# Optimization experiments

Hardware: AMD Instinct MI355X
Metric: run time of the kernel (lower is better)

Reference implementation:

```python
import jax, jax.numpy as jnp
import numpy as np
from jax import lax

DN = ('NCHW', 'OIHW', 'NCHW')


def convbn(x, w, s, b, relu=True):
    # conv (no bias) + folded BatchNorm affine (+ optional ReLU)
    y = lax.conv_general_dilated(x, w, (1, 1), 'SAME', dimension_numbers=DN)
    y = y * s[None, :, None, None] + b[None, :, None, None]
    return jnp.maximum(y, 0.0) if relu else y


_PARAM_SHAPES = [
    ('t', (128, 256, 3, 3)), ('l', (128, 256, 3, 3)),
    ('b', (128, 256, 3, 3)), ('r', (128, 256, 3, 3)),
    ('tl3', (256, 128, 3, 3)), ('br3', (256, 128, 3, 3)),
    ('tl1', (256, 256, 1, 1)), ('br1', (256, 256, 1, 1)),
    ('tlo', (256, 256, 3, 3)), ('bro', (256, 256, 3, 3)),
]


def setup_inputs() -> dict:
    key = jax.random.key(0)
    B, C, H, W = 8, 256, 128, 128
    ks = jax.random.split(key, 3 * len(_PARAM_SHAPES) + 1)
    inp = {'x': jax.random.normal(ks[0], (B, C, H, W), jnp.float32)}
    i = 1
    for name, shape in _PARAM_SHAPES:
        cout = shape[0]
        inp['w_' + name] = jax.random.normal(ks[i], shape, jnp.float32) * 0.05
        inp['s_' + name] = 1.0 + 0.1 * jax.random.normal(ks[i + 1], (cout,), jnp.float32)
        inp['b_' + name] = 0.1 * jax.random.normal(ks[i + 2], (cout,), jnp.float32)
        i += 3
    return inp


def reference(x, w_t, s_t, b_t, w_l, s_l, b_l, w_b, s_b, b_b, w_r, s_r, b_r,
              w_tl3, s_tl3, b_tl3, w_br3, s_br3, b_br3,
              w_tl1, s_tl1, b_tl1, w_br1, s_br1, b_br1,
              w_tlo, s_tlo, b_tlo, w_bro, s_bro, b_bro):
    # directional corner pools = (reverse-)cummax along H (axis 2) or W (axis 3)
    t = convbn(x, w_t, s_t, b_t)
    tp = lax.cummax(t, axis=2, reverse=True)   # top_pool: max over rows >= h
    l = convbn(x, w_l, s_l, b_l)
    lp = lax.cummax(l, axis=3, reverse=True)   # left_pool: max over cols >= w
    bo = convbn(x, w_b, s_b, b_b)
    bp = lax.cummax(bo, axis=2)                # bottom_pool: max over rows <= h
    r = convbn(x, w_r, s_r, b_r)
    rp = lax.cummax(r, axis=3)                 # right_pool: max over cols <= w

    tl = convbn(tp + lp, w_tl3, s_tl3, b_tl3, relu=False)
    tl = jnp.maximum(tl + convbn(x, w_tl1, s_tl1, b_tl1, relu=False), 0.0)
    out_tl = convbn(tl, w_tlo, s_tlo, b_tlo)

    br = convbn(bp + rp, w_br3, s_br3, b_br3, relu=False)
    br = jnp.maximum(br + convbn(x, w_br1, s_br1, b_br1, relu=False), 0.0)
    out_br = convbn(br, w_bro, s_bro, b_bro)
    return out_tl, out_br
```

## Files before the change

### kernel.cpp

```cpp
#include <hip/hip_runtime.h>
#include <cstdint>
#include <cstddef>


typedef float  f32x4 __attribute__((ext_vector_type(4)));
typedef float  f4v   __attribute__((ext_vector_type(4)));
typedef short  s16x8 __attribute__((ext_vector_type(8)));
typedef unsigned short u16x4 __attribute__((ext_vector_type(4)));

__device__ __forceinline__ float bf2f(unsigned short u) {
    unsigned x = ((unsigned)u) << 16;
    return __builtin_bit_cast(float, x);
}
__device__ __forceinline__ unsigned short f2bf(float f) {
    unsigned u = __builtin_bit_cast(unsigned, f);
    unsigned r = (u + 0x7fffu + ((u >> 16) & 1u)) >> 16;
    return (unsigned short)r;
}

#define GL_LDS(gp, lp) __builtin_amdgcn_global_load_lds( \
    (const __attribute__((address_space(1))) unsigned int*)(const void*)(gp), \
    (__attribute__((address_space(3))) unsigned int*)(void*)(lp), 16, 0, 0)

template<int CIN, int COUT, bool RELU, bool OUTF32>
__global__ __launch_bounds__(256, 4)
void conv3_mfma(const unsigned short* __restrict__ in,
                const unsigned short* __restrict__ wpk,
                const float* __restrict__ sc, const float* __restrict__ bi,
                void* __restrict__ outv)
{
    __shared__ unsigned short lds[2][8704];
    const int tid  = threadIdx.x;
    const int lane = tid & 63;
    const int wv   = tid >> 6;
    const int c    = lane & 15;
    const int g    = lane >> 4;
    const int gx     = blockIdx.x;
    const int wtile  = gx & 1;
    const int octile = gx >> 1;
    const int h0   = blockIdx.y * 2;
    const int n    = blockIdx.z;
    const int w0   = wtile * 64;
    const int r    = wv >> 1;
    const int ocbase = octile * 128 + (wv & 1) * 64;
    const int ocf0   = octile * 8 + (wv & 1) * 4;

    int addrB[3];
    #pragma unroll
    for (int kx = 0; kx < 3; ++kx) {
        int ps0 = c + kx;
        addrB[kx] = r * 4224 + ps0 * 64 + ((g ^ ((ps0 >> 1) & 3)) << 4);
    }

    int so[5];
    #pragma unroll
    for (int it = 0; it < 5; ++it) {
        int u   = it * 256 + tid;
        int row = u / 264;
        int rem = u - row * 264;
        int ps  = rem >> 2;
        int s   = rem & 3;
        int icq = s ^ ((ps >> 1) & 3);
        so[it] = ((n * 130 + h0 + row) * 130 + (w0 + ps)) * CIN + icq * 8;
    }

    auto STAGE = [&](int chunk, int bsel) {
        const unsigned short* bp = in + chunk * 32;
        char* lb = (char*)lds + bsel * 17408 + tid * 16;
        #pragma unroll
        for (int it = 0; it < 4; ++it)
            GL_LDS(bp + so[it], lb + it * 4096);
        if (wv == 0)
            GL_LDS(bp + so[4], lb + 16384);
    };

    f32x4 acc[4][4];
    #pragma unroll
    for (int m = 0; m < 4; ++m)
        #pragma unroll
        for (int p = 0; p < 4; ++p) acc[m][p] = 0.0f;

    const int NC = CIN / 32;
    STAGE(0, 0);
    __syncthreads();

    for (int chunk = 0; chunk < NC; ++chunk) {
        const int cur = chunk & 1;
        if (chunk + 1 < NC) STAGE(chunk + 1, cur ^ 1);
        const char* lb = (const char*)lds + cur * 17408;
        #pragma unroll
        for (int kk = 0; kk < 9; ++kk) {
            const int ky = kk / 3, kx = kk % 3;
            s16x8 af[4], bf[4];
            #pragma unroll
            for (int m = 0; m < 4; ++m)
                af[m] = *(const s16x8*)(wpk
                    + ((size_t)((chunk * 9 + kk) * (COUT / 16) + ocf0 + m)) * 512 + lane * 8);
            #pragma unroll
            for (int p = 0; p < 4; ++p)
                bf[p] = *(const s16x8*)(lb + addrB[kx] + ky * 4224 + p * 1024);
            #pragma unroll
            for (int m = 0; m < 4; ++m)
                #pragma unroll
                for (int p = 0; p < 4; ++p)
                    acc[m][p] = __builtin_amdgcn_mfma_f32_16x16x32_bf16(af[m], bf[p], acc[m][p], 0, 0, 0);
        }
        __syncthreads();
    }

    #pragma unroll
    for (int m = 0; m < 4; ++m) {
        const int oc4 = ocbase + m * 16 + g * 4;
        const f4v s4 = *(const f4v*)(sc + oc4);
        const f4v b4 = *(const f4v*)(bi + oc4);
        #pragma unroll
        for (int p = 0; p < 4; ++p) {
            const int w = w0 + p * 16 + c;
            float y[4];
            #pragma unroll
            for (int j = 0; j < 4; ++j) {
                y[j] = acc[m][p][j] * s4[j] + b4[j];
                if (RELU) y[j] = fmaxf(y[j], 0.0f);
            }
            if (OUTF32) {
                float* op = (float*)outv + (((size_t)n * COUT + oc4) << 14) + ((h0 + r) << 7) + w;
                op[0] = y[0]; op[16384] = y[1]; op[32768] = y[2]; op[49152] = y[3];
            } else {
                u16x4 pk;
                #pragma unroll
                for (int j = 0; j < 4; ++j) pk[j] = f2bf(y[j]);
                *(u16x4*)((unsigned short*)outv
                    + ((size_t)(n * 130 + h0 + r + 1) * 130 + w + 1) * COUT + oc4) = pk;
            }
        }
    }
}

__global__ __launch_bounds__(256, 2)
void conv1_mfma(const unsigned short* __restrict__ xb,
                const unsigned short* __restrict__ w1pk,
                const float* __restrict__ sc, const float* __restrict__ bi,
                unsigned short* __restrict__ io)
{
    const int tid  = threadIdx.x;
    const int h    = blockIdx.y;
    const int n    = blockIdx.z;
    const int lane = tid & 63;
    const int wv   = tid >> 6;
    const int c    = lane & 15;
    const int g    = lane >> 4;
    const int pixbase = (wv >> 1) * 64;
    const int ocbase  = blockIdx.x * 128 + (wv & 1) * 64;
    const int ocf0    = blockIdx.x * 8 + (wv & 1) * 4;
    const size_t pixrow = ((size_t)(n * 130 + h + 1) * 130 + (pixbase + c + 1)) * 256;

    f32x4 acc[4][4];
    #pragma unroll
    for (int m = 0; m < 4; ++m)
        #pragma unroll
        for (int p = 0; p < 4; ++p) acc[m][p] = 0.0f;

    s16x8 a0[4], b0[4], a1[4], b1[4];

#define LOADC(ck, A, B) do {                                                        \
    _Pragma("unroll") for (int p = 0; p < 4; ++p)                                   \
        B[p] = *(const s16x8*)(xb + pixrow + (size_t)(16 * p) * 256 + (ck) * 32 + g * 8); \
    _Pragma("unroll") for (int m = 0; m < 4; ++m)                                   \
        A[m] = *(const s16x8*)(w1pk + ((size_t)((ck) * 16 + ocf0 + m)) * 512 + lane * 8); \
} while (0)
#define MM(A, B)                                                                    \
    _Pragma("unroll") for (int m = 0; m < 4; ++m)                                   \
        _Pragma("unroll") for (int p = 0; p < 4; ++p)                               \
            acc[m][p] = __builtin_amdgcn_mfma_f32_16x16x32_bf16(A[m], B[p], acc[m][p], 0, 0, 0)

    LOADC(0, a0, b0);
    #pragma unroll
    for (int ck = 0; ck < 8; ++ck) {
        if ((ck & 1) == 0) { if (ck < 7) LOADC(ck + 1, a1, b1); MM(a0, b0); }
        else               { if (ck < 7) LOADC(ck + 1, a0, b0); MM(a1, b1); }
    }
#undef LOADC
#undef MM

    #pragma unroll
    for (int m = 0; m < 4; ++m) {
        const int oc4 = ocbase + m * 16 + g * 4;
        const f4v s4 = *(const f4v*)(sc + oc4);
        const f4v b4 = *(const f4v*)(bi + oc4);
        #pragma unroll
        for (int p = 0; p < 4; ++p) {
            const int pix = pixbase + p * 16 + c;
            size_t idx = ((size_t)(n * 130 + h + 1) * 130 + pix + 1) * 256 + oc4;
            u16x4 old = *(const u16x4*)(io + idx);
            u16x4 pk;
            #pragma unroll
            for (int j = 0; j < 4; ++j) {
                float y = acc[m][p][j] * s4[j] + b4[j] + bf2f(old[j]);
                pk[j] = f2bf(fmaxf(y, 0.0f));
            }
            *(u16x4*)(io + idx) = pk;
        }
    }
}

template<bool REV>
__global__ __launch_bounds__(128)
void pool_h_k(unsigned short* __restrict__ p)
{
    const int n = blockIdx.x >> 7, w = blockIdx.x & 127, cth = threadIdx.x;
    unsigned short* base = p + (((size_t)n * 130 + 1) * 130 + (w + 1)) * 128 + cth;
    const int stride = 130 * 128;
    float m = -3.402823466e+38f;
    for (int i = 0; i < 128; ++i) {
        int hh = REV ? (127 - i) : i;
        unsigned short* q = base + (size_t)hh * stride;
        m = fmaxf(m, bf2f(*q));
        *q = f2bf(m);
    }
}

template<bool REV>
__global__ __launch_bounds__(128)
void pool_w_add_k(const unsigned short* __restrict__ lsrc,
                  unsigned short* __restrict__ tdst)
{
    const int n = blockIdx.x >> 7, hh = blockIdx.x & 127, cth = threadIdx.x;
    const size_t rowbase = ((size_t)(n * 130 + hh + 1) * 130) * 128 + cth;
    float m = -3.402823466e+38f;
    for (int i = 0; i < 128; ++i) {
        int w = REV ? (127 - i) : i;
        size_t off = rowbase + (size_t)(w + 1) * 128;
        m = fmaxf(m, bf2f(lsrc[off]));
        tdst[off] = f2bf(m + bf2f(tdst[off]));
    }
}

__global__ __launch_bounds__(256)
void padzero_k(unsigned short* __restrict__ t, int C)
{
    int idx = blockIdx.x * 256 + threadIdx.x;
    int n = blockIdx.y;
    int cpu = C >> 3;
    if (idx >= 516 * cpu) return;
    int cell = idx / cpu, cq = idx - cell * cpu;
    int h, w;
    if (cell < 260) { h = (cell < 130) ? -1 : 128; w = (cell % 130) - 1; }
    else { int j = cell - 260; w = (j < 128) ? -1 : 128; h = j & 127; }
    size_t off = (((size_t)n * 130 + h + 1) * 130 + (w + 1)) * C + cq * 8;
    uint4 z; z.x = 0; z.y = 0; z.z = 0; z.w = 0;
    *(uint4*)(t + off) = z;
}

__global__ __launch_bounds__(256)
void transform_x_k(const float* __restrict__ x, unsigned short* __restrict__ xb)
{
    __shared__ float sm[64][132];
    const int h = blockIdx.x, n = blockIdx.y, t = threadIdx.x;
    for (int cc0 = 0; cc0 < 256; cc0 += 64) {
        __syncthreads();
        {
            int ci = t >> 7, wi = t & 127;
            #pragma unroll 8
            for (int k = 0; k < 32; ++k)
                sm[ci + 2 * k][wi] = x[((size_t)(n * 256 + cc0 + ci + 2 * k) << 14) + (h << 7) + wi];
        }
        __syncthreads();
        {
            int wi = t >> 1, cq = t & 1;
            unsigned short tmp[32];
            #pragma unroll
            for (int m2 = 0; m2 < 32; ++m2) tmp[m2] = f2bf(sm[cq * 32 + m2][wi]);
            unsigned short* dst = xb + (((size_t)n * 130 + h + 1) * 130 + wi + 1) * 256 + cc0 + cq * 32;
            #pragma unroll
            for (int q = 0; q < 4; ++q) *(uint4*)(dst + q * 8) = *(const uint4*)(tmp + q * 8);
        }
    }
}

__global__ __launch_bounds__(256)
void prepack3_k(const float* __restrict__ w, unsigned short* __restrict__ dst,
                int CIN, int COUT)
{
    int idx = blockIdx.x * 256 + threadIdx.x;
    if (idx >= COUT * CIN * 9) return;
    int kk = idx % 9; int rest = idx / 9;
    int ic = rest % CIN; int oc = rest / CIN;
    float v = w[(size_t)(oc * CIN + ic) * 9 + kk];
    int chunk = ic >> 5, icr = ic & 31, gg = icr >> 3, j = icr & 7;
    int m = oc >> 4, ocr = oc & 15, ln = gg * 16 + ocr;
    size_t off = ((size_t)((chunk * 9 + kk) * (COUT / 16) + m)) * 512 + ln * 8 + j;
    dst[off] = f2bf(v);
}

__global__ __launch_bounds__(256)
void prepack1_k(const float* __restrict__ w, unsigned short* __restrict__ dst)
{
    int idx = blockIdx.x * 256 + threadIdx.x;
    if (idx >= 65536) return;
    int ic = idx & 255, oc = idx >> 8;
    float v = w[oc * 256 + ic];
    int chunk = ic >> 5, icr = ic & 31, gg = icr >> 3, j = icr & 7;
    int m = oc >> 4, ocr = oc & 15, ln = gg * 16 + ocr;
    size_t off = ((size_t)(chunk * 16 + m)) * 512 + ln * 8 + j;
    dst[off] = f2bf(v);
}

extern "C" void kernel_launch(void* const* d_in, const int* in_sizes, int n_in,
                              void* d_out, int out_size, void* d_ws, size_t ws_size,
                              hipStream_t stream)
{
    const float* x     = (const float*)d_in[0];
    const float* w_t   = (const float*)d_in[1];
    const float* s_t   = (const float*)d_in[2];
    const float* b_t   = (const float*)d_in[3];
    const float* w_l   = (const float*)d_in[4];
    const float* s_l   = (const float*)d_in[5];
    const float* b_l   = (const float*)d_in[6];
    const float* w_b   = (const float*)d_in[7];
    const float* s_b   = (const float*)d_in[8];
    const float* b_b   = (const float*)d_in[9];
    const float* w_r   = (const float*)d_in[10];
    const float* s_r   = (const float*)d_in[11];
    const float* b_r   = (const float*)d_in[12];
    const float* w_tl3 = (const float*)d_in[13];
    const float* s_tl3 = (const float*)d_in[14];
    const float* b_tl3 = (const float*)d_in[15];
    const float* w_br3 = (const float*)d_in[16];
    const float* s_br3 = (const float*)d_in[17];
    const float* b_br3 = (const float*)d_in[18];
    const float* w_tl1 = (const float*)d_in[19];
    const float* s_tl1 = (const float*)d_in[20];
    const float* b_tl1 = (const float*)d_in[21];
    const float* w_br1 = (const float*)d_in[22];
    const float* s_br1 = (const float*)d_in[23];
    const float* b_br1 = (const float*)d_in[24];
    const float* w_tlo = (const float*)d_in[25];
    const float* s_tlo = (const float*)d_in[26];
    const float* b_tlo = (const float*)d_in[27];
    const float* w_bro = (const float*)d_in[28];
    const float* s_bro = (const float*)d_in[29];
    const float* b_bro = (const float*)d_in[30];

    typedef unsigned short ush;
    const size_t T256 = (size_t)8 * 130 * 130 * 256;
    const size_t T128 = (size_t)8 * 130 * 130 * 128;

    ush* xb = (ush*)d_ws;
    ush* tt = xb + T256;
    ush* bb = tt + T128;
    ush* ll = bb + T128;
    ush* rr = ll + T128;
    ush* wq = rr + T128;
    ush* wp_t   = wq;
    ush* wp_l   = wp_t   + 294912;
    ush* wp_b   = wp_l   + 294912;
    ush* wp_r   = wp_b   + 294912;
    ush* wp_tl3 = wp_r   + 294912;
    ush* wp_br3 = wp_tl3 + 294912;
    ush* wp_tlo = wp_br3 + 294912;
    ush* wp_bro = wp_tlo + 589824;
    ush* wp_tl1 = wp_bro + 589824;
    ush* wp_br1 = wp_tl1 + 65536;
    ush* tl = ll;

    prepack3_k<<<dim3((294912 + 255) / 256), dim3(256), 0, stream>>>(w_t,   wp_t,   256, 128);
    prepack3_k<<<dim3((294912 + 255) / 256), dim3(256), 0, stream>>>(w_l,   wp_l,   256, 128);
    prepack3_k<<<dim3((294912 + 255) / 256), dim3(256), 0, stream>>>(w_b,   wp_b,   256, 128);
    prepack3_k<<<dim3((294912 + 255) / 256), dim3(256), 0, stream>>>(w_r,   wp_r,   256, 128);
    prepack3_k<<<dim3((294912 + 255) / 256), dim3(256), 0, stream>>>(w_tl3, wp_tl3, 128, 256);
    prepack3_k<<<dim3((294912 + 255) / 256), dim3(256), 0, stream>>>(w_br3, wp_br3, 128, 256);
    prepack3_k<<<dim3((589824 + 255) / 256), dim3(256), 0, stream>>>(w_tlo, wp_tlo, 256, 256);
    prepack3_k<<<dim3((589824 + 255) / 256), dim3(256), 0, stream>>>(w_bro, wp_bro, 256, 256);
    prepack1_k<<<dim3(256), dim3(256), 0, stream>>>(w_tl1, wp_tl1);
    prepack1_k<<<dim3(256), dim3(256), 0, stream>>>(w_br1, wp_br1);

    padzero_k<<<dim3(66, 8), dim3(256), 0, stream>>>(xb, 256);
    padzero_k<<<dim3(33, 8), dim3(256), 0, stream>>>(tt, 128);
    padzero_k<<<dim3(33, 8), dim3(256), 0, stream>>>(bb, 128);
    padzero_k<<<dim3(33, 8), dim3(256), 0, stream>>>(ll, 128);
    padzero_k<<<dim3(33, 8), dim3(256), 0, stream>>>(rr, 128);

    transform_x_k<<<dim3(128, 8), dim3(256), 0, stream>>>(x, xb);

    conv3_mfma<256, 128, true, false><<<dim3(2, 64, 8), dim3(256), 0, stream>>>(xb, wp_t, s_t, b_t, tt);
    conv3_mfma<256, 128, true, false><<<dim3(2, 64, 8), dim3(256), 0, stream>>>(xb, wp_l, s_l, b_l, ll);
    conv3_mfma<256, 128, true, false><<<dim3(2, 64, 8), dim3(256), 0, stream>>>(xb, wp_b, s_b, b_b, bb);
    conv3_mfma<256, 128, true, false><<<dim3(2, 64, 8), dim3(256), 0, stream>>>(xb, wp_r, s_r, b_r, rr);

    pool_h_k<true ><<<dim3(1024), dim3(128), 0, stream>>>(tt);
    pool_h_k<false><<<dim3(1024), dim3(128), 0, stream>>>(bb);
    pool_w_add_k<true ><<<dim3(1024), dim3(128), 0, stream>>>(ll, tt);
    pool_w_add_k<false><<<dim3(1024), dim3(128), 0, stream>>>(rr, bb);

    padzero_k<<<dim3(66, 8), dim3(256), 0, stream>>>(tl, 256);
    conv3_mfma<128, 256, false, false><<<dim3(4, 64, 8), dim3(256), 0, stream>>>(tt, wp_tl3, s_tl3, b_tl3, tl);
    conv1_mfma<<<dim3(2, 128, 8), dim3(256), 0, stream>>>(xb, wp_tl1, s_tl1, b_tl1, tl);
    conv3_mfma<256, 256, true, true><<<dim3(4, 64, 8), dim3(256), 0, stream>>>(tl, wp_tlo, s_tlo, b_tlo, d_out);

    conv3_mfma<128, 256, false, false><<<dim3(4, 64, 8), dim3(256), 0, stream>>>(bb, wp_br3, s_br3, b_br3, tl);
    conv1_mfma<<<dim3(2, 128, 8), dim3(256), 0, stream>>>(xb, wp_br1, s_br1, b_br1, tl);
    conv3_mfma<256, 256, true, true><<<dim3(4, 64, 8), dim3(256), 0, stream>>>(tl, wp_bro, s_bro, b_bro,
                                                                               (float*)d_out + 33554432);
}
```

Baseline: 1.046 ms.

## Add XCD-aware block swizzle to convs and merge pool kernels into paired launches

Adds a compile-time option to the 3x3 conv kernel that remaps the linear block index so consecutive work-groups on each of the 8 XCDs cover contiguous output tiles, aiming for better L2 reuse. It is enabled on half of the conv launches, apparently as an A/B comparison. The four directional pool kernels become two launches that each handle both tensors, and their loops are batched in groups of 8 loads before the stores to expose memory-level parallelism. The cost is more index arithmetic, and enabling swizzling on only some launches is inconsistent.

```diff
diff --git a/kernel.cpp b/kernel.cpp
--- a/kernel.cpp
+++ b/kernel.cpp
@@ -22,7 +22,7 @@
     (const __attribute__((address_space(1))) unsigned int*)(const void*)(gp), \
     (__attribute__((address_space(3))) unsigned int*)(void*)(lp), 16, 0, 0)
 
-template<int CIN, int COUT, bool RELU, bool OUTF32>
+template<int CIN, int COUT, bool RELU, bool OUTF32, bool SWZ>
 __global__ __launch_bounds__(256, 4)
 void conv3_mfma(const unsigned short* __restrict__ in,
                 const unsigned short* __restrict__ wpk,
@@ -35,11 +35,24 @@
     const int wv   = tid >> 6;
     const int c    = lane & 15;
     const int g    = lane >> 4;
-    const int gx     = blockIdx.x;
+
+    constexpr int GX  = (COUT / 128) * 2;
+    int gx, hy, n;
+    if (SWZ) {
+        constexpr int NWG = GX * 64 * 8;
+        constexpr int Q   = NWG / 8;
+        const int braw = blockIdx.x + GX * (blockIdx.y + 64 * blockIdx.z);
+        const int wl   = (braw & 7) * Q + (braw >> 3);
+        gx = wl % GX;
+        const int rest = wl / GX;
+        hy = rest & 63;
+        n  = rest >> 6;
+    } else {
+        gx = blockIdx.x; hy = blockIdx.y; n = blockIdx.z;
+    }
     const int wtile  = gx & 1;
     const int octile = gx >> 1;
-    const int h0   = blockIdx.y * 2;
-    const int n    = blockIdx.z;
+    const int h0   = hy * 2;
     const int w0   = wtile * 64;
     const int r    = wv >> 1;
     const int ocbase = octile * 128 + (wv & 1) * 64;
@@ -203,35 +216,84 @@
     }
 }
 
-template<bool REV>
 __global__ __launch_bounds__(128)
-void pool_h_k(unsigned short* __restrict__ p)
-{
-    const int n = blockIdx.x >> 7, w = blockIdx.x & 127, cth = threadIdx.x;
+void pool_h2_k(unsigned short* __restrict__ ta, unsigned short* __restrict__ tb)
+{
+    const int sel = blockIdx.x & 1;
+    const int col = blockIdx.x >> 1;
+    unsigned short* p = sel ? tb : ta;
+    const int n = col >> 7, w = col & 127, cth = threadIdx.x;
     unsigned short* base = p + (((size_t)n * 130 + 1) * 130 + (w + 1)) * 128 + cth;
     const int stride = 130 * 128;
     float m = -3.402823466e+38f;
-    for (int i = 0; i < 128; ++i) {
-        int hh = REV ? (127 - i) : i;
-        unsigned short* q = base + (size_t)hh * stride;
-        m = fmaxf(m, bf2f(*q));
-        *q = f2bf(m);
-    }
-}
-
-template<bool REV>
+    if (sel == 0) {
+        for (int gq = 0; gq < 16; ++gq) {
+            const int h0 = 127 - gq * 8;
+            float v[8];
+            #pragma unroll
+            for (int j = 0; j < 8; ++j) v[j] = bf2f(base[(size_t)(h0 - j) * stride]);
+            unsigned short o[8];
+            #pragma unroll
+            for (int j = 0; j < 8; ++j) { m = fmaxf(m, v[j]); o[j] = f2bf(m); }
+            #pragma unroll
+            for (int j = 0; j < 8; ++j) base[(size_t)(h0 - j) * stride] = o[j];
+        }
+    } else {
+        for (int gq = 0; gq < 16; ++gq) {
+            const int h0 = gq * 8;
+            float v[8];
+            #pragma unroll
+            for (int j = 0; j < 8; ++j) v[j] = bf2f(base[(size_t)(h0 + j) * stride]);
+            unsigned short o[8];
+            #pragma unroll
+            for (int j = 0; j < 8; ++j) { m = fmaxf(m, v[j]); o[j] = f2bf(m); }
+            #pragma unroll
+            for (int j = 0; j < 8; ++j) base[(size_t)(h0 + j) * stride] = o[j];
+        }
+    }
+}
+
 __global__ __launch_bounds__(128)
-void pool_w_add_k(const unsigned short* __restrict__ lsrc,
-                  unsigned short* __restrict__ tdst)
-{
-    const int n = blockIdx.x >> 7, hh = blockIdx.x & 127, cth = threadIdx.x;
+void pool_w_add2_k(const unsigned short* __restrict__ la, unsigned short* __restrict__ ta,
+                   const unsigned short* __restrict__ lb, unsigned short* __restrict__ tb)
+{
+    const int sel = blockIdx.x & 1;
+    const int row = blockIdx.x >> 1;
+    const unsigned short* ls = sel ? lb : la;
+    unsigned short* td = sel ? tb : ta;
+    const int n = row >> 7, hh = row & 127, cth = threadIdx.x;
     const size_t rowbase = ((size_t)(n * 130 + hh + 1) * 130) * 128 + cth;
     float m = -3.402823466e+38f;
-    for (int i = 0; i < 128; ++i) {
-        int w = REV ? (127 - i) : i;
-        size_t off = rowbase + (size_t)(w + 1) * 128;
-        m = fmaxf(m, bf2f(lsrc[off]));
-        tdst[off] = f2bf(m + bf2f(tdst[off]));
+    if (sel == 0) {
+        for (int gq = 0; gq < 16; ++gq) {
+            const int w0 = 127 - gq * 8;
+            float lv[8], tv[8];
+            #pragma unroll
+            for (int j = 0; j < 8; ++j) {
+                size_t off = rowbase + (size_t)(w0 - j + 1) * 128;
+                lv[j] = bf2f(ls[off]); tv[j] = bf2f(td[off]);
+            }
+            unsigned short o[8];
+            #pragma unroll
+            for (int j = 0; j < 8; ++j) { m = fmaxf(m, lv[j]); o[j] = f2bf(m + tv[j]); }
+            #pragma unroll
+            for (int j = 0; j < 8; ++j) td[rowbase + (size_t)(w0 - j + 1) * 128] = o[j];
+        }
+    } else {
+        for (int gq = 0; gq < 16; ++gq) {
+            const int w0 = gq * 8;
+            float lv[8], tv[8];
+            #pragma unroll
+            for (int j = 0; j < 8; ++j) {
+                size_t off = rowbase + (size_t)(w0 + j + 1) * 128;
+                lv[j] = bf2f(ls[off]); tv[j] = bf2f(td[off]);
+            }
+            unsigned short o[8];
+            #pragma unroll
+            for (int j = 0; j < 8; ++j) { m = fmaxf(m, lv[j]); o[j] = f2bf(m + tv[j]); }
+            #pragma unroll
+            for (int j = 0; j < 8; ++j) td[rowbase + (size_t)(w0 + j + 1) * 128] = o[j];
+        }
     }
 }
 
@@ -382,23 +444,21 @@
 
     transform_x_k<<<dim3(128, 8), dim3(256), 0, stream>>>(x, xb);
 
-    conv3_mfma<256, 128, true, false><<<dim3(2, 64, 8), dim3(256), 0, stream>>>(xb, wp_t, s_t, b_t, tt);
-    conv3_mfma<256, 128, true, false><<<dim3(2, 64, 8), dim3(256), 0, stream>>>(xb, wp_l, s_l, b_l, ll);
-    conv3_mfma<256, 128, true, false><<<dim3(2, 64, 8), dim3(256), 0, stream>>>(xb, wp_b, s_b, b_b, bb);
-    conv3_mfma<256, 128, true, false><<<dim3(2, 64, 8), dim3(256), 0, stream>>>(xb, wp_r, s_r, b_r, rr);
-
-    pool_h_k<true ><<<dim3(1024), dim3(128), 0, stream>>>(tt);
-    pool_h_k<false><<<dim3(1024), dim3(128), 0, stream>>>(bb);
-    pool_w_add_k<true ><<<dim3(1024), dim3(128), 0, stream>>>(ll, tt);
-    pool_w_add_k<false><<<dim3(1024), dim3(128), 0, stream>>>(rr, bb);
+    conv3_mfma<256, 128, true, false, true ><<<dim3(2, 64, 8), dim3(256), 0, stream>>>(xb, wp_t, s_t, b_t, tt);
+    conv3_mfma<256, 128, true, false, true ><<<dim3(2, 64, 8), dim3(256), 0, stream>>>(xb, wp_l, s_l, b_l, ll);
+    conv3_mfma<256, 128, true, false, false><<<dim3(2, 64, 8), dim3(256), 0, stream>>>(xb, wp_b, s_b, b_b, bb);
+    conv3_mfma<256, 128, true, false, false><<<dim3(2, 64, 8), dim3(256), 0, stream>>>(xb, wp_r, s_r, b_r, rr);
+
+    pool_h2_k<<<dim3(2048), dim3(128), 0, stream>>>(tt, bb);
+    pool_w_add2_k<<<dim3(2048), dim3(128), 0, stream>>>(ll, tt, rr, bb);
 
     padzero_k<<<dim3(66, 8), dim3(256), 0, stream>>>(tl, 256);
-    conv3_mfma<128, 256, false, false><<<dim3(4, 64, 8), dim3(256), 0, stream>>>(tt, wp_tl3, s_tl3, b_tl3, tl);
+    conv3_mfma<128, 256, false, false, true ><<<dim3(4, 64, 8), dim3(256), 0, stream>>>(tt, wp_tl3, s_tl3, b_tl3, tl);
     conv1_mfma<<<dim3(2, 128, 8), dim3(256), 0, stream>>>(xb, wp_tl1, s_tl1, b_tl1, tl);
-    conv3_mfma<256, 256, true, true><<<dim3(4, 64, 8), dim3(256), 0, stream>>>(tl, wp_tlo, s_tlo, b_tlo, d_out);
-
-    conv3_mfma<128, 256, false, false><<<dim3(4, 64, 8), dim3(256), 0, stream>>>(bb, wp_br3, s_br3, b_br3, tl);
+    conv3_mfma<256, 256, true, true, true ><<<dim3(4, 64, 8), dim3(256), 0, stream>>>(tl, wp_tlo, s_tlo, b_tlo, d_out);
+
+    conv3_mfma<128, 256, false, false, false><<<dim3(4, 64, 8), dim3(256), 0, stream>>>(bb, wp_br3, s_br3, b_br3, tl);
     conv1_mfma<<<dim3(2, 128, 8), dim3(256), 0, stream>>>(xb, wp_br1, s_br1, b_br1, tl);
-    conv3_mfma<256, 256, true, true><<<dim3(4, 64, 8), dim3(256), 0, stream>>>(tl, wp_bro, s_bro, b_bro,
-                                                                               (float*)d_out + 33554432);
-}
+    conv3_mfma<256, 256, true, true, false><<<dim3(4, 64, 8), dim3(256), 0, stream>>>(tl, wp_bro, s_bro, b_bro,
+                                                                                      (float*)d_out + 33554432);
+}
```

Measured after the change: 1.002 ms. 1.04x faster.
